# Kernel optimization log

Hardware: AMD Instinct MI355X
Metric: run time of the kernel (lower is better)

## Reference

```python
import jax, jax.numpy as jnp
import numpy as np

N, E, F, R, S = 20000, 320000, 64, 8, 10
AVG_NEIGH = 16.0


def setup_inputs() -> dict:
    key = jax.random.key(0)
    ks = jax.random.split(key, 16)
    inp = {
        "vectors": jax.random.normal(ks[0], (E, 3), jnp.float32),
        "node_feats": jax.random.normal(ks[1], (N, F, 4), jnp.float32),  # [N, F, 1(0e)+3(1o)]
        "node_specie": jax.random.randint(ks[2], (N,), 0, S),
        "radial_embedding": jax.random.normal(ks[3], (E, R), jnp.float32),
        "senders": jax.random.randint(ks[4], (E,), 0, N),
        "receivers": jax.random.randint(ks[5], (E,), 0, N),
        # residual FullyConnectedTensorProduct(feats, one-hot species 0e) == species-dep. linear per l
        "W_res_s": jax.random.normal(ks[6], (S, F, F), jnp.float32),
        "W_res_v": jax.random.normal(ks[7], (S, F, F), jnp.float32),
        # interaction block: input linear per l
        "W_in_s": jax.random.normal(ks[8], (F, F), jnp.float32),
        "W_in_v": jax.random.normal(ks[9], (F, F), jnp.float32),
        # radial MLP -> 5 CG tensor-product path weights per channel
        "mlp_w1": jax.random.normal(ks[10], (R, 64), jnp.float32),
        "mlp_w2": jax.random.normal(ks[11], (64, 5 * F), jnp.float32) / 8.0,
        # interaction block: output linear per l
        "W_out_s": jax.random.normal(ks[12], (F, F), jnp.float32),
        "W_out_v": jax.random.normal(ks[13], (F, F), jnp.float32),
        # symmetric product basis (correlation 3), species-dependent term weights
        "W_prod_s": jax.random.normal(ks[14], (S, 5, F), jnp.float32) * 0.3,
        "W_prod_v": jax.random.normal(ks[15], (S, 4, F), jnp.float32) * 0.3,
    }
    k2 = jax.random.split(jax.random.key(1), 3)
    inp["W_lin_s"] = jax.random.normal(k2[0], (F, F), jnp.float32)
    inp["W_lin_v"] = jax.random.normal(k2[1], (F, F), jnp.float32)
    inp["W_read"] = jax.random.normal(k2[2], (F, 1), jnp.float32)
    return inp


def _forward(vectors, node_feats, node_specie, radial_embedding, senders, receivers,
             W_res_s, W_res_v, W_in_s, W_in_v, mlp_w1, mlp_w2, W_out_s, W_out_v,
             W_prod_s, W_prod_v, W_lin_s, W_lin_v, W_read):
    inv_sf = 1.0 / jnp.sqrt(jnp.float32(F))
    s = node_feats[..., 0]          # [N,F]   0e channels
    v = node_feats[..., 1:]         # [N,F,3] 1o channels

    # --- residual connection: FCTP(feats, one-hot species 0e attrs) -> species-gated linear per l
    res_s = jnp.einsum('nf,ngf->ng', s, W_res_s[node_specie]) * inv_sf
    res_v = jnp.einsum('nfc,ngf->ngc', v, W_res_v[node_specie]) * inv_sf

    # --- InteractionBlock ---
    h_s = (s @ W_in_s) * inv_sf
    h_v = jnp.einsum('nfc,fg->ngc', v, W_in_v) * inv_sf

    # spherical harmonics up to max_ell=1: Y0 = 1, Y1 = unit edge vector
    r = jnp.sqrt(jnp.sum(vectors * vectors, -1) + 1e-12)
    Y1 = vectors / r[:, None]                                # [E,3]

    # radial MLP produces per-edge weights for the 5 CG paths:
    # (0e x Y0 -> 0e), (1o . Y1 -> 0e), (0e x Y1 -> 1o), (1o x Y0 -> 1o), (1o x Y1 -> 1o, cross)
    w = (jax.nn.silu(radial_embedding @ mlp_w1) @ mlp_w2).reshape(-1, 5, F)  # [E,5,F]

    ss = h_s[senders]                                        # [E,F]
    sv = h_v[senders]                                        # [E,F,3]
    dot = jnp.einsum('efc,ec->ef', sv, Y1)                   # [E,F]
    m_s = w[:, 0] * ss + w[:, 1] * dot                       # [E,F]
    m_v = (w[:, 2] * ss)[:, :, None] * Y1[:, None, :] \
        + w[:, 3][:, :, None] * sv \
        + w[:, 4][:, :, None] * jnp.cross(sv, Y1[:, None, :])  # [E,F,3]

    agg_s = jnp.zeros_like(h_s).at[receivers].add(m_s) / AVG_NEIGH
    agg_v = jnp.zeros_like(h_v).at[receivers].add(m_v) / AVG_NEIGH
    a_s = (agg_s @ W_out_s) * inv_sf
    a_v = jnp.einsum('nfc,fg->ngc', agg_v, W_out_v) * inv_sf

    # --- EquivariantProductBasisBlock: correlation-3 symmetric contraction, species-dependent ---
    vv = jnp.sum(a_v * a_v, -1)                              # [N,F] invariant |v|^2
    Wp = W_prod_s[node_specie]                               # [N,5,F]
    p_s = (Wp[:, 0] * a_s + Wp[:, 1] * a_s ** 2 + Wp[:, 2] * a_s ** 3
           + Wp[:, 3] * vv + Wp[:, 4] * a_s * vv)
    Wv = W_prod_v[node_specie]                               # [N,4,F]
    p_v = (Wv[:, 0] + Wv[:, 1] * a_s + Wv[:, 2] * a_s ** 2 + Wv[:, 3] * vv)[:, :, None] * a_v

    f_s = (p_s @ W_lin_s) * inv_sf + res_s
    f_v = jnp.einsum('nfc,fg->ngc', p_v, W_lin_v) * inv_sf + res_v

    # --- LinearReadoutBlock (output_irreps = 0e), 1 head ---
    node_out = ((f_s @ W_read) * inv_sf)[:, None, :]         # [N, heads=1, 1]
    new_feats = jnp.concatenate([f_s[..., None], f_v], axis=-1)  # [N,F,4]
    return node_out, new_feats


def reference(vectors, node_feats, node_specie, radial_embedding, senders, receivers,
              W_res_s, W_res_v, W_in_s, W_in_v, mlp_w1, mlp_w2, W_out_s, W_out_v,
              W_prod_s, W_prod_v, W_lin_s, W_lin_v, W_read):
    return _forward(vectors, node_feats, node_specie, radial_embedding, senders, receivers,
                    W_res_s, W_res_v, W_in_s, W_in_v, mlp_w1, mlp_w2, W_out_s, W_out_v,
                    W_prod_s, W_prod_v, W_lin_s, W_lin_v, W_read)
```

## Files before the change

kernel.cpp:

```cpp
#include <hip/hip_runtime.h>
#include <math.h>

#define NN 20000
#define NE 320000
#define NF (NN*64)
#define TB 16

typedef float v2f __attribute__((ext_vector_type(2)));

#if __has_builtin(__builtin_elementwise_fma)
#define PKFMA(a,b,c) __builtin_elementwise_fma(a,b,c)
#else
static __device__ __forceinline__ v2f PKFMA(v2f a, v2f b, v2f c){
  v2f r; r.x = fmaf(a.x,b.x,c.x); r.y = fmaf(a.y,b.y,c.y); return r;
}
#endif

__global__ __launch_bounds__(256) void k_pre(
    const float* __restrict__ node_feats, const float* __restrict__ W_in_s,
    const float* __restrict__ W_in_v, float* __restrict__ h,
    const int* __restrict__ receivers, int* __restrict__ count, int* __restrict__ rank,
    const float* __restrict__ Ws, const float* __restrict__ Wv,
    float* __restrict__ Wst, float* __restrict__ Wvt,
    const float* __restrict__ w2, float* __restrict__ w2r)
{
  __shared__ float sh[16][4][64];
  if(blockIdx.x >= 1250){
    int b = blockIdx.x - 1250;
    int e = b*256 + threadIdx.x;
    rank[e] = atomicAdd(&count[receivers[e]], 1);
    if(b < 160){
      int i = b*256 + threadIdx.x;
      int spec = i >> 12;
      int g = (i >> 6) & 63;
      int f = i & 63;
      Wst[spec*4096 + f*64 + g] = Ws[i];
      Wvt[spec*4096 + f*64 + g] = Wv[i];
    } else if(b < 288){
      int i = (b-160)*256 + threadIdx.x;
      int hh = i >> 9;
      int r  = i & 511;
      int ln = r >> 3;
      int j  = r & 7;
      w2r[i] = (j < 5) ? w2[hh*320 + j*64 + ln] : 0.f;
    }
    return;
  }
  int wave = threadIdx.x >> 6, lane = threadIdx.x & 63;
  int nb = blockIdx.x*16 + wave*4;
  #pragma unroll
  for(int k=0;k<4;++k){
    int nd = wave*4 + k;
    float4 nf = *(const float4*)(node_feats + (size_t)((nb+k)*64 + lane)*4);
    sh[nd][0][lane]=nf.x; sh[nd][1][lane]=nf.y; sh[nd][2][lane]=nf.z; sh[nd][3][lane]=nf.w;
  }
  __syncthreads();
  float as[4]={0,0,0,0}, a0[4]={0,0,0,0}, a1[4]={0,0,0,0}, a2[4]={0,0,0,0};
  for(int f=0; f<64; ++f){
    float ws = W_in_s[f*64+lane], wv = W_in_v[f*64+lane];
    #pragma unroll
    for(int k=0;k<4;++k){
      int nd = wave*4 + k;
      as[k] = fmaf(sh[nd][0][f], ws, as[k]);
      a0[k] = fmaf(sh[nd][1][f], wv, a0[k]);
      a1[k] = fmaf(sh[nd][2][f], wv, a1[k]);
      a2[k] = fmaf(sh[nd][3][f], wv, a2[k]);
    }
  }
  #pragma unroll
  for(int k=0;k<4;++k){
    float4 o4; o4.x = as[k]*0.125f; o4.y = a0[k]*0.125f;
    o4.z = a1[k]*0.125f; o4.w = a2[k]*0.125f;
    *(float4*)(h + (size_t)((nb+k)*64 + lane)*4) = o4;
  }
}

__global__ __launch_bounds__(1024) void k_scan(const int* __restrict__ count,
                                               int* __restrict__ offset)
{
  __shared__ int part[1024];
  int t = threadIdx.x;
  const int PER = 20;
  int base = t*PER;
  int loc[PER];
  int s = 0;
  #pragma unroll
  for(int i=0;i<PER;++i){
    int idx = base+i;
    int v = (idx < NN) ? count[idx] : 0;
    loc[i] = v; s += v;
  }
  part[t] = s;
  __syncthreads();
  for(int off=1; off<1024; off<<=1){
    int v = (t>=off) ? part[t-off] : 0;
    __syncthreads();
    part[t] += v;
    __syncthreads();
  }
  int run = t ? part[t-1] : 0;
  #pragma unroll
  for(int i=0;i<PER;++i){
    int idx = base+i;
    if(idx < NN) offset[idx] = run;
    run += loc[i];
  }
  if(t==1023) offset[NN] = part[1023];
}

__global__ __launch_bounds__(256) void k_scatter(
    const int* __restrict__ senders, const int* __restrict__ receivers,
    const float* __restrict__ vectors, const float* __restrict__ radial,
    const int* __restrict__ offset, const int* __restrict__ rank,
    float* __restrict__ rec)
{
  int e = blockIdx.x*256 + threadIdx.x;
  int r = receivers[e];
  int slot = offset[r] + rank[e];
  float vx = vectors[e*3], vy = vectors[e*3+1], vz = vectors[e*3+2];
  float rinv = rsqrtf(vx*vx + vy*vy + vz*vz + 1e-12f);
  float4 ra = *(const float4*)(radial + (size_t)e*8);
  float4 rb = *(const float4*)(radial + (size_t)e*8 + 4);
  float* rp = rec + (size_t)slot*16;
  float4 w0; w0.x = vx*rinv; w0.y = vy*rinv; w0.z = vz*rinv; w0.w = __int_as_float(senders[e]);
  float4 w3; w3.x = __int_as_float(r); w3.y = 0.f; w3.z = 0.f; w3.w = 0.f;
  *(float4*)(rp)      = w0;
  *(float4*)(rp + 4)  = ra;
  *(float4*)(rp + 8)  = rb;
  *(float4*)(rp + 12) = w3;
}

__global__ __launch_bounds__(256) void k_edge(
    const float* __restrict__ rec,
    const float* __restrict__ mlp_w1, const float* __restrict__ mlp_w2,
    const float* __restrict__ h, float* __restrict__ agg)
{
  __shared__ float recS[4][256];
  __shared__ float hid[4][64][20];
  int tid = threadIdx.x;
  int wave = tid >> 6, lane = tid & 63;
  int e0 = (blockIdx.x*4 + wave)*TB;

  *(float4*)&recS[wave][lane*4] = *(const float4*)(rec + (size_t)e0*16 + lane*4);

  float wl[8];
  #pragma unroll
  for(int r=0;r<8;++r) wl[r] = mlp_w1[r*64+lane];

  #pragma unroll
  for(int t=0;t<TB;++t){
    float acc = 0.f;
    #pragma unroll
    for(int r=0;r<8;++r) acc = fmaf(recS[wave][t*16+4+r], wl[r], acc);
    hid[wave][lane][t] = acc / (1.f + __expf(-acc));
  }

  v2f wv[5][8];
  #pragma unroll
  for(int j=0;j<5;++j)
    #pragma unroll
    for(int tp=0;tp<8;++tp) wv[j][tp] = (v2f){0.f, 0.f};
  const float* w2p = mlp_w2 + lane;
  for(int hh=0; hh<64; ++hh){
    float b[5];
    #pragma unroll
    for(int j=0;j<5;++j) b[j] = w2p[hh*320 + j*64];
    v2f hv[8];
    #pragma unroll
    for(int tp=0;tp<8;++tp) hv[tp] = *(const v2f*)&hid[wave][hh][2*tp];
    #pragma unroll
    for(int j=0;j<5;++j){
      v2f bb = {b[j], b[j]};
      #pragma unroll
      for(int tp=0;tp<8;++tp) wv[j][tp] = PKFMA(bb, hv[tp], wv[j][tp]);
    }
  }

  float4 hv4[4];
  #pragma unroll
  for(int p=0;p<4;++p){
    int snd = __float_as_int(recS[wave][p*16+3]);
    hv4[p] = *(const float4*)(h + (size_t)(snd*64 + lane)*4);
  }

  float as_=0.f, av0=0.f, av1=0.f, av2=0.f;
  int cur = __float_as_int(recS[wave][12]);
  #pragma unroll
  for(int t=0;t<TB;++t){
    float4 hc = hv4[t&3];
    if(t+4 < TB){
      int snd = __float_as_int(recS[wave][(t+4)*16+3]);
      hv4[t&3] = *(const float4*)(h + (size_t)(snd*64 + lane)*4);
    }
    int rcv = __float_as_int(recS[wave][t*16+12]);
    if(rcv != cur){
      size_t ro = (size_t)cur*256 + lane;
      atomicAdd(&agg[ro],     as_);
      atomicAdd(&agg[ro+64],  av0);
      atomicAdd(&agg[ro+128], av1);
      atomicAdd(&agg[ro+192], av2);
      as_=0.f; av0=0.f; av1=0.f; av2=0.f;
      cur = rcv;
    }
    float y0=recS[wave][t*16], y1=recS[wave][t*16+1], y2=recS[wave][t*16+2];
    float ss=hc.x, sv0=hc.y, sv1=hc.z, sv2=hc.w;
    float dot = sv0*y0 + sv1*y1 + sv2*y2;
    float wt0 = wv[0][t>>1][t&1], wt1 = wv[1][t>>1][t&1];
    float wt2 = wv[2][t>>1][t&1], wt3 = wv[3][t>>1][t&1], wt4 = wv[4][t>>1][t&1];
    as_ += wt0*ss + wt1*dot;
    float w2s = wt2*ss;
    av0 += w2s*y0 + wt3*sv0 + wt4*(sv1*y2 - sv2*y1);
    av1 += w2s*y1 + wt3*sv1 + wt4*(sv2*y0 - sv0*y2);
    av2 += w2s*y2 + wt3*sv2 + wt4*(sv0*y1 - sv1*y0);
  }
  size_t ro = (size_t)cur*256 + lane;
  atomicAdd(&agg[ro],     as_);
  atomicAdd(&agg[ro+64],  av0);
  atomicAdd(&agg[ro+128], av1);
  atomicAdd(&agg[ro+192], av2);
}

__global__ __launch_bounds__(256) void k_node_post(
  const float* __restrict__ node_feats, const int* __restrict__ specie,
  const float* __restrict__ agg,
  const float* __restrict__ Wrst, const float* __restrict__ Wrvt,
  const float* __restrict__ W_out_s, const float* __restrict__ W_out_v,
  const float* __restrict__ W_prod_s, const float* __restrict__ W_prod_v,
  const float* __restrict__ W_lin_s, const float* __restrict__ W_lin_v,
  const float* __restrict__ W_read, float* __restrict__ out_node,
  float* __restrict__ out_feats)
{
  __shared__ float shA[16][4][64];
  __shared__ float shS[16][4][64];
  int wave = threadIdx.x >> 6, lane = threadIdx.x & 63;
  int nb = blockIdx.x*16 + wave*4;
  #pragma unroll
  for(int k=0;k<4;++k){
    int nd = wave*4 + k;
    size_t o = (size_t)(nb+k)*256 + lane;
    shA[nd][0][lane] = agg[o]      * (1.f/16.f);
    shA[nd][1][lane] = agg[o+64]   * (1.f/16.f);
    shA[nd][2][lane] = agg[o+128]  * (1.f/16.f);
    shA[nd][3][lane] = agg[o+192]  * (1.f/16.f);
    float4 nf = *(const float4*)(node_feats + (size_t)((nb+k)*64 + lane)*4);
    shS[nd][0][lane]=nf.x; shS[nd][1][lane]=nf.y; shS[nd][2][lane]=nf.z; shS[nd][3][lane]=nf.w;
  }
  int spec[4];
  #pragma unroll
  for(int k=0;k<4;++k) spec[k] = specie[nb+k];
  __syncthreads();
  float a_s[4]={0,0,0,0}, a0[4]={0,0,0,0}, a1[4]={0,0,0,0}, a2[4]={0,0,0,0};
  float r_s[4]={0,0,0,0}, r0[4]={0,0,0,0}, r1[4]={0,0,0,0}, r2[4]={0,0,0,0};
  for(int f=0; f<64; ++f){
    float wos = W_out_s[f*64+lane], wov = W_out_v[f*64+lane];
    #pragma unroll
    for(int k=0;k<4;++k){
      int nd = wave*4 + k;
      a_s[k] = fmaf(shA[nd][0][f], wos, a_s[k]);
      a0[k]  = fmaf(shA[nd][1][f], wov, a0[k]);
      a1[k]  = fmaf(shA[nd][2][f], wov, a1[k]);
      a2[k]  = fmaf(shA[nd][3][f], wov, a2[k]);
    }
    #pragma unroll
    for(int k=0;k<4;++k){
      int nd = wave*4 + k;
      float wrs = Wrst[spec[k]*4096 + f*64 + lane];
      float wrv = Wrvt[spec[k]*4096 + f*64 + lane];
      r_s[k] = fmaf(shS[nd][0][f], wrs, r_s[k]);
      r0[k]  = fmaf(shS[nd][1][f], wrv, r0[k]);
      r1[k]  = fmaf(shS[nd][2][f], wrv, r1[k]);
      r2[k]  = fmaf(shS[nd][3][f], wrv, r2[k]);
    }
  }
  __syncthreads();
  #pragma unroll
  for(int k=0;k<4;++k){
    int nd = wave*4 + k;
    float A_s = a_s[k]*0.125f, A0 = a0[k]*0.125f, A1 = a1[k]*0.125f, A2 = a2[k]*0.125f;
    float vv = A0*A0 + A1*A1 + A2*A2;
    float as2 = A_s*A_s;
    const float* Wp = W_prod_s + spec[k]*320;
    float p_s = Wp[lane]*A_s + Wp[64+lane]*as2 + Wp[128+lane]*as2*A_s
              + Wp[192+lane]*vv + Wp[256+lane]*A_s*vv;
    const float* Wq = W_prod_v + spec[k]*256;
    float coef = Wq[lane] + Wq[64+lane]*A_s + Wq[128+lane]*as2 + Wq[192+lane]*vv;
    shS[nd][0][lane] = p_s;
    shS[nd][1][lane] = coef*A0;
    shS[nd][2][lane] = coef*A1;
    shS[nd][3][lane] = coef*A2;
  }
  __syncthreads();
  float lfs[4]={0,0,0,0}, lf0[4]={0,0,0,0}, lf1[4]={0,0,0,0}, lf2[4]={0,0,0,0};
  for(int f=0; f<64; ++f){
    float wls = W_lin_s[f*64+lane], wlv = W_lin_v[f*64+lane];
    #pragma unroll
    for(int k=0;k<4;++k){
      int nd = wave*4 + k;
      lfs[k] = fmaf(shS[nd][0][f], wls, lfs[k]);
      lf0[k] = fmaf(shS[nd][1][f], wlv, lf0[k]);
      lf1[k] = fmaf(shS[nd][2][f], wlv, lf1[k]);
      lf2[k] = fmaf(shS[nd][3][f], wlv, lf2[k]);
    }
  }
  float wr = W_read[lane];
  #pragma unroll
  for(int k=0;k<4;++k){
    int n = nb + k;
    float FS = lfs[k]*0.125f + r_s[k]*0.125f;
    float F0 = lf0[k]*0.125f + r0[k]*0.125f;
    float F1 = lf1[k]*0.125f + r1[k]*0.125f;
    float F2 = lf2[k]*0.125f + r2[k]*0.125f;
    float x = FS * wr;
    #pragma unroll
    for(int off=32; off; off>>=1) x += __shfl_down(x, off);
    if(lane==0) out_node[n] = x*0.125f;
    float4 o4; o4.x=FS; o4.y=F0; o4.z=F1; o4.w=F2;
    *(float4*)(out_feats + (size_t)(n*64+lane)*4) = o4;
  }
}

extern "C" void kernel_launch(void* const* d_in, const int* in_sizes, int n_in,
                              void* d_out, int out_size, void* d_ws, size_t ws_size,
                              hipStream_t stream) {
  const float* vectors    = (const float*)d_in[0];
  const float* node_feats = (const float*)d_in[1];
  const int*   node_specie= (const int*)  d_in[2];
  const float* radial     = (const float*)d_in[3];
  const int*   senders    = (const int*)  d_in[4];
  const int*   receivers  = (const int*)  d_in[5];
  const float* W_res_s    = (const float*)d_in[6];
  const float* W_res_v    = (const float*)d_in[7];
  const float* W_in_s     = (const float*)d_in[8];
  const float* W_in_v     = (const float*)d_in[9];
  const float* mlp_w1     = (const float*)d_in[10];
  const float* mlp_w2     = (const float*)d_in[11];
  const float* W_out_s    = (const float*)d_in[12];
  const float* W_out_v    = (const float*)d_in[13];
  const float* W_prod_s   = (const float*)d_in[14];
  const float* W_prod_v   = (const float*)d_in[15];
  const float* W_lin_s    = (const float*)d_in[16];
  const float* W_lin_v    = (const float*)d_in[17];
  const float* W_read     = (const float*)d_in[18];

  float* ws   = (float*)d_ws;
  float* h    = ws;
  float* agg  = ws + 4*(size_t)NF;
  float* Wrst = ws + 8*(size_t)NF;
  float* Wrvt = Wrst + 40960;
  float* rec  = Wrvt + 40960;
  float* w2r  = rec + 16*(size_t)NE;
  int*   rank   = (int*)(w2r + 32768);
  int*   offset = rank + NE;
  int*   count  = offset + NN + 1;

  hipMemsetAsync(agg,   0, (size_t)4*NF*sizeof(float), stream);
  hipMemsetAsync(count, 0, (size_t)NN*sizeof(int), stream);
  k_pre<<<2500, 256, 0, stream>>>(node_feats, W_in_s, W_in_v, h,
                                  receivers, count, rank,
                                  W_res_s, W_res_v, Wrst, Wrvt,
                                  mlp_w2, w2r);
  k_scan   <<<1,     1024, 0, stream>>>(count, offset);
  k_scatter<<<NE/256, 256, 0, stream>>>(senders, receivers, vectors, radial,
                                        offset, rank, rec);
  k_edge<<<NE/64, 256, 0, stream>>>(rec, mlp_w1, mlp_w2, h, agg);
  k_node_post<<<NN/16, 256, 0, stream>>>(node_feats, node_specie, agg,
                                         Wrst, Wrvt, W_out_s, W_out_v,
                                         W_prod_s, W_prod_v, W_lin_s, W_lin_v,
                                         W_read, (float*)d_out, (float*)d_out + NN);
}
```

Measured before the change: 446.1 us.

## Sort nodes by species so node_post blocks share residual weight rows

Counts and ranks nodes per species with atomics, scans the species offsets, builds a species-sorted node permutation, and has k_node_post process nodes in that order. Nodes in a block then mostly share the same species, so the species-dependent residual weight loads (Wrst/Wrvt) hit the same addresses and cache better. In exchange, per-node loads of agg and node_feats and the output stores become scattered, and a small amount of extra preprocessing is added. The atomic ranking makes the order within a species nondeterministic, but the results are not affected.

New measurement: 502.4 us. 1.13x slower.

```diff
diff --git a/kernel.cpp b/kernel.cpp
--- a/kernel.cpp
+++ b/kernel.cpp
@@ -22,7 +22,8 @@
     const int* __restrict__ receivers, int* __restrict__ count, int* __restrict__ rank,
     const float* __restrict__ Ws, const float* __restrict__ Wv,
     float* __restrict__ Wst, float* __restrict__ Wvt,
-    const float* __restrict__ w2, float* __restrict__ w2r)
+    const float* __restrict__ w2, float* __restrict__ w2r,
+    const int* __restrict__ specie, int* __restrict__ scount, int* __restrict__ srank)
 {
   __shared__ float sh[16][4][64];
   if(blockIdx.x >= 1250){
@@ -43,6 +44,9 @@
       int ln = r >> 3;
       int j  = r & 7;
       w2r[i] = (j < 5) ? w2[hh*320 + j*64 + ln] : 0.f;
+    } else if(b < 367){
+      int n2 = (b-288)*256 + threadIdx.x;
+      if(n2 < NN) srank[n2] = atomicAdd(&scount[specie[n2]], 1);
     }
     return;
   }
@@ -76,10 +80,16 @@
 }
 
 __global__ __launch_bounds__(1024) void k_scan(const int* __restrict__ count,
-                                               int* __restrict__ offset)
+                                               int* __restrict__ offset,
+                                               const int* __restrict__ scount,
+                                               int* __restrict__ soffset)
 {
   __shared__ int part[1024];
   int t = threadIdx.x;
+  if(t == 0){
+    int run = 0;
+    for(int s=0;s<10;++s){ soffset[s] = run; run += scount[s]; }
+  }
   const int PER = 20;
   int base = t*PER;
   int loc[PER];
@@ -112,8 +122,14 @@
     const int* __restrict__ senders, const int* __restrict__ receivers,
     const float* __restrict__ vectors, const float* __restrict__ radial,
     const int* __restrict__ offset, const int* __restrict__ rank,
-    float* __restrict__ rec)
-{
+    float* __restrict__ rec,
+    const int* __restrict__ specie, const int* __restrict__ soffset,
+    const int* __restrict__ srank, int* __restrict__ norder)
+{
+  if(blockIdx.x < 79){
+    int n2 = blockIdx.x*256 + threadIdx.x;
+    if(n2 < NN) norder[soffset[specie[n2]] + srank[n2]] = n2;
+  }
   int e = blockIdx.x*256 + threadIdx.x;
   int r = receivers[e];
   int slot = offset[r] + rank[e];
@@ -222,7 +238,7 @@
 
 __global__ __launch_bounds__(256) void k_node_post(
   const float* __restrict__ node_feats, const int* __restrict__ specie,
-  const float* __restrict__ agg,
+  const float* __restrict__ agg, const int* __restrict__ norder,
   const float* __restrict__ Wrst, const float* __restrict__ Wrvt,
   const float* __restrict__ W_out_s, const float* __restrict__ W_out_v,
   const float* __restrict__ W_prod_s, const float* __restrict__ W_prod_v,
@@ -234,20 +250,23 @@
   __shared__ float shS[16][4][64];
   int wave = threadIdx.x >> 6, lane = threadIdx.x & 63;
   int nb = blockIdx.x*16 + wave*4;
+  int nk[4];
+  #pragma unroll
+  for(int k=0;k<4;++k) nk[k] = norder[nb+k];
   #pragma unroll
   for(int k=0;k<4;++k){
     int nd = wave*4 + k;
-    size_t o = (size_t)(nb+k)*256 + lane;
+    size_t o = (size_t)nk[k]*256 + lane;
     shA[nd][0][lane] = agg[o]      * (1.f/16.f);
     shA[nd][1][lane] = agg[o+64]   * (1.f/16.f);
     shA[nd][2][lane] = agg[o+128]  * (1.f/16.f);
     shA[nd][3][lane] = agg[o+192]  * (1.f/16.f);
-    float4 nf = *(const float4*)(node_feats + (size_t)((nb+k)*64 + lane)*4);
+    float4 nf = *(const float4*)(node_feats + (size_t)(nk[k]*64 + lane)*4);
     shS[nd][0][lane]=nf.x; shS[nd][1][lane]=nf.y; shS[nd][2][lane]=nf.z; shS[nd][3][lane]=nf.w;
   }
   int spec[4];
   #pragma unroll
-  for(int k=0;k<4;++k) spec[k] = specie[nb+k];
+  for(int k=0;k<4;++k) spec[k] = specie[nk[k]];
   __syncthreads();
   float a_s[4]={0,0,0,0}, a0[4]={0,0,0,0}, a1[4]={0,0,0,0}, a2[4]={0,0,0,0};
   float r_s[4]={0,0,0,0}, r0[4]={0,0,0,0}, r1[4]={0,0,0,0}, r2[4]={0,0,0,0};
@@ -305,7 +324,7 @@
   float wr = W_read[lane];
   #pragma unroll
   for(int k=0;k<4;++k){
-    int n = nb + k;
+    int n = nk[k];
     float FS = lfs[k]*0.125f + r_s[k]*0.125f;
     float F0 = lf0[k]*0.125f + r0[k]*0.125f;
     float F1 = lf1[k]*0.125f + r1[k]*0.125f;
@@ -352,18 +371,24 @@
   int*   rank   = (int*)(w2r + 32768);
   int*   offset = rank + NE;
   int*   count  = offset + NN + 1;
+  int*   scount = count + NN;
+  int*   soffset= scount + 16;
+  int*   srank  = soffset + 16;
+  int*   norder = srank + NN;
 
   hipMemsetAsync(agg,   0, (size_t)4*NF*sizeof(float), stream);
-  hipMemsetAsync(count, 0, (size_t)NN*sizeof(int), stream);
+  hipMemsetAsync(count, 0, (size_t)(NN+16)*sizeof(int), stream);
   k_pre<<<2500, 256, 0, stream>>>(node_feats, W_in_s, W_in_v, h,
                                   receivers, count, rank,
                                   W_res_s, W_res_v, Wrst, Wrvt,
-                                  mlp_w2, w2r);
-  k_scan   <<<1,     1024, 0, stream>>>(count, offset);
+                                  mlp_w2, w2r,
+                                  node_specie, scount, srank);
+  k_scan   <<<1,     1024, 0, stream>>>(count, offset, scount, soffset);
   k_scatter<<<NE/256, 256, 0, stream>>>(senders, receivers, vectors, radial,
-                                        offset, rank, rec);
+                                        offset, rank, rec,
+                                        node_specie, soffset, srank, norder);
   k_edge<<<NE/64, 256, 0, stream>>>(rec, mlp_w1, mlp_w2, h, agg);
-  k_node_post<<<NN/16, 256, 0, stream>>>(node_feats, node_specie, agg,
+  k_node_post<<<NN/16, 256, 0, stream>>>(node_feats, node_specie, agg, norder,
                                          Wrst, Wrvt, W_out_s, W_out_v,
                                          W_prod_s, W_prod_v, W_lin_s, W_lin_v,
                                          W_read, (float*)d_out, (float*)d_out + NN);
```
